# Kernel optimization log

Hardware: AMD Instinct MI355X
Metric: run time of the kernel (lower is better)

The kernel has to match this reference:

```python
import jax, jax.numpy as jnp
import numpy as np
from jax import lax

SIGMA = 1.5
KERNEL_SIZE = 11
C1 = 0.01 ** 2  # (k1 * data_range)^2 with data_range = 1.0
C2 = 0.03 ** 2


def _gaussian_kernel_1d(kernel_size: int, sigma: float) -> jnp.ndarray:
    coords = jnp.arange(kernel_size, dtype=jnp.float32) - (kernel_size - 1) / 2.0
    g = jnp.exp(-(coords ** 2) / (2.0 * sigma ** 2))
    return g / jnp.sum(g)


def _gaussian_blur(x: jnp.ndarray, g: jnp.ndarray) -> jnp.ndarray:
    """Separable depthwise Gaussian blur, VALID padding. x: [B,C,H,W], g: [k]."""
    c = x.shape[1]
    k = g.shape[0]
    dn = lax.conv_dimension_numbers(x.shape, (c, 1, k, 1), ('NCHW', 'OIHW', 'NCHW'))
    wh = jnp.broadcast_to(g.reshape(1, 1, k, 1), (c, 1, k, 1)).astype(x.dtype)
    ww = jnp.broadcast_to(g.reshape(1, 1, 1, k), (c, 1, 1, k)).astype(x.dtype)
    y = lax.conv_general_dilated(x, wh, (1, 1), 'VALID', dimension_numbers=dn, feature_group_count=c)
    y = lax.conv_general_dilated(y, ww, (1, 1), 'VALID', dimension_numbers=dn, feature_group_count=c)
    return y


def setup_inputs() -> dict:
    key = jax.random.key(0)
    k1, k2 = jax.random.split(key)
    shape = (16, 3, 512, 512)
    return {
        'input': jax.random.uniform(k1, shape, dtype=jnp.float32),
        'target': jax.random.uniform(k2, shape, dtype=jnp.float32),
    }


def reference(input, target):
    g = _gaussian_kernel_1d(KERNEL_SIZE, SIGMA)
    mu_x = _gaussian_blur(input, g)
    mu_y = _gaussian_blur(target, g)
    mu_x2 = mu_x * mu_x
    mu_y2 = mu_y * mu_y
    mu_xy = mu_x * mu_y
    var_x = _gaussian_blur(input * input, g) - mu_x2
    var_y = _gaussian_blur(target * target, g) - mu_y2
    cov_xy = _gaussian_blur(input * target, g) - mu_xy
    ssim_map = ((2.0 * mu_xy + C1) * (2.0 * cov_xy + C2)) / ((mu_x2 + mu_y2 + C1) * (var_x + var_y + C2))
    return 1.0 - jnp.mean(ssim_map)
```

## Files before the change

### kernel.cpp

```cpp
#include <hip/hip_runtime.h>

#define IH 512
#define IW 512
#define OH 502
#define OW 502
#define KS 11
#define HO 16
#define NSTRIP 32
#define NCH 48
#define NBLK (NCH * NSTRIP)
#define NT 256
#define LROW 528
#define C1f 0.0001f
#define C2f 0.0009f

__device__ __constant__ float g_w[KS] = {
    0.00102838f, 0.00759876f, 0.03600077f, 0.10936069f, 0.21300554f,
    0.26601173f, 0.21300554f, 0.10936069f, 0.03600077f, 0.00759876f,
    0.00102838f};

#define BARRIER() do {                                        \
    asm volatile("s_waitcnt lgkmcnt(0)" ::: "memory");        \
    __builtin_amdgcn_s_barrier();                             \
} while (0)

__global__ __launch_bounds__(NT, 2) void ssim_main(const float* __restrict__ x,
                                                   const float* __restrict__ y,
                                                   double* __restrict__ acc,
                                                   unsigned int* __restrict__ cnt,
                                                   float* __restrict__ out) {
    __shared__ float lds[5][2][LROW];
    __shared__ float red[4];

    const int t = threadIdx.x;
    const int ch = blockIdx.x / NSTRIP;
    const int strip = blockIdx.x % NSTRIP;
    const int r0 = strip * HO;
    const float* __restrict__ xc = x + (size_t)ch * IH * IW + 2 * t;
    const float* __restrict__ yc = y + (size_t)ch * IH * IW + 2 * t;

    float2 rx[KS], ry[KS];
#pragma unroll
    for (int i = 0; i < KS; ++i) {
        const int gr = min(r0 + i, IH - 1);
        rx[i] = *(const float2*)(xc + gr * IW);
        ry[i] = *(const float2*)(yc + gr * IW);
    }
    float2 nx0, ny0, nx1, ny1;
    {
        const int g0 = min(r0 + 11, IH - 1);
        const int g1 = min(r0 + 12, IH - 1);
        nx0 = *(const float2*)(xc + g0 * IW);
        ny0 = *(const float2*)(yc + g0 * IW);
        nx1 = *(const float2*)(xc + g1 * IW);
        ny1 = *(const float2*)(yc + g1 * IW);
    }

    float lsum = 0.f;

    for (int k = 0; k < HO / 2; ++k) {
        {
            float s0[2] = {0.f, 0.f}, s1[2] = {0.f, 0.f}, s2[2] = {0.f, 0.f};
            float s3[2] = {0.f, 0.f}, s4[2] = {0.f, 0.f};
#pragma unroll
            for (int tp = 0; tp < KS; ++tp) {
                const float w = g_w[tp];
                const float2 xv = rx[tp];
                const float2 yv = ry[tp];
                const float wx0 = w * xv.x, wx1 = w * xv.y;
                const float wy0 = w * yv.x, wy1 = w * yv.y;
                s0[0] += wx0;  s0[1] += wx1;
                s1[0] += wy0;  s1[1] += wy1;
                s2[0] = fmaf(wx0, xv.x, s2[0]);  s2[1] = fmaf(wx1, xv.y, s2[1]);
                s3[0] = fmaf(wy0, yv.x, s3[0]);  s3[1] = fmaf(wy1, yv.y, s3[1]);
                s4[0] = fmaf(wx0, yv.x, s4[0]);  s4[1] = fmaf(wx1, yv.y, s4[1]);
            }
            *(float2*)&lds[0][0][2 * t] = make_float2(s0[0], s0[1]);
            *(float2*)&lds[1][0][2 * t] = make_float2(s1[0], s1[1]);
            *(float2*)&lds[2][0][2 * t] = make_float2(s2[0], s2[1]);
            *(float2*)&lds[3][0][2 * t] = make_float2(s3[0], s3[1]);
            *(float2*)&lds[4][0][2 * t] = make_float2(s4[0], s4[1]);
        }
        {
            float s0[2] = {0.f, 0.f}, s1[2] = {0.f, 0.f}, s2[2] = {0.f, 0.f};
            float s3[2] = {0.f, 0.f}, s4[2] = {0.f, 0.f};
#pragma unroll
            for (int tp = 0; tp < KS; ++tp) {
                const float w = g_w[tp];
                const float2 xv = (tp < KS - 1) ? rx[tp + 1] : nx0;
                const float2 yv = (tp < KS - 1) ? ry[tp + 1] : ny0;
                const float wx0 = w * xv.x, wx1 = w * xv.y;
                const float wy0 = w * yv.x, wy1 = w * yv.y;
                s0[0] += wx0;  s0[1] += wx1;
                s1[0] += wy0;  s1[1] += wy1;
                s2[0] = fmaf(wx0, xv.x, s2[0]);  s2[1] = fmaf(wx1, xv.y, s2[1]);
                s3[0] = fmaf(wy0, yv.x, s3[0]);  s3[1] = fmaf(wy1, yv.y, s3[1]);
                s4[0] = fmaf(wx0, yv.x, s4[0]);  s4[1] = fmaf(wx1, yv.y, s4[1]);
            }
            *(float2*)&lds[0][1][2 * t] = make_float2(s0[0], s0[1]);
            *(float2*)&lds[1][1][2 * t] = make_float2(s1[0], s1[1]);
            *(float2*)&lds[2][1][2 * t] = make_float2(s2[0], s2[1]);
            *(float2*)&lds[3][1][2 * t] = make_float2(s3[0], s3[1]);
            *(float2*)&lds[4][1][2 * t] = make_float2(s4[0], s4[1]);
        }
        BARRIER();

#pragma unroll
        for (int i = 0; i < KS - 2; ++i) { rx[i] = rx[i + 2]; ry[i] = ry[i + 2]; }
        rx[KS - 2] = nx0; ry[KS - 2] = ny0;
        rx[KS - 1] = nx1; ry[KS - 1] = ny1;
        {
            const int g0 = min(r0 + 2 * k + 13, IH - 1);
            const int g1 = min(r0 + 2 * k + 14, IH - 1);
            nx0 = *(const float2*)(xc + g0 * IW);
            ny0 = *(const float2*)(yc + g0 * IW);
            nx1 = *(const float2*)(xc + g1 * IW);
            ny1 = *(const float2*)(yc + g1 * IW);
        }

        {
            const int rr = t >> 7;
            const int c4 = (t & 127) * 4;
            const int orow = r0 + 2 * k + rr;
            float m[5][4];
#pragma unroll
            for (int q = 0; q < 5; ++q) {
                float f[16];
#pragma unroll
                for (int a = 0; a < 4; ++a)
                    *(float4*)&f[4 * a] = *(const float4*)&lds[q][rr][c4 + 4 * a];
#pragma unroll
                for (int cc = 0; cc < 4; ++cc) {
                    float s = 0.f;
#pragma unroll
                    for (int tp = 0; tp < KS; ++tp) s = fmaf(g_w[tp], f[cc + tp], s);
                    m[q][cc] = s;
                }
            }
            if (orow < OH) {
#pragma unroll
                for (int cc = 0; cc < 4; ++cc) {
                    const int gc = c4 + cc;
                    if (gc < OW) {
                        const float mux2 = m[0][cc] * m[0][cc];
                        const float muy2 = m[1][cc] * m[1][cc];
                        const float muxy = m[0][cc] * m[1][cc];
                        const float vx = m[2][cc] - mux2;
                        const float vy = m[3][cc] - muy2;
                        const float cxy = m[4][cc] - muxy;
                        const float num = (2.f * muxy + C1f) * (2.f * cxy + C2f);
                        const float den = (mux2 + muy2 + C1f) * (vx + vy + C2f);
                        float r = __builtin_amdgcn_rcpf(den);
                        r = r * fmaf(-den, r, 2.0f);
                        lsum = fmaf(num, r, lsum);
                    }
                }
            }
        }
        BARRIER();
    }

#pragma unroll
    for (int off = 32; off > 0; off >>= 1) lsum += __shfl_down(lsum, off, 64);
    const int wave = t >> 6, lane = t & 63;
    if (lane == 0) red[wave] = lsum;
    __syncthreads();
    if (t == 0) {
        const float bs = (red[0] + red[1]) + (red[2] + red[3]);
        atomicAdd(acc, (double)bs);
        __threadfence();
        const unsigned int prev = atomicAdd(cnt, 1u);
        if (prev == (unsigned int)(NBLK - 1)) {
            const double total = atomicAdd(acc, 0.0);
            out[0] = (float)(1.0 - total / 12096192.0);
        }
    }
}

extern "C" void kernel_launch(void* const* d_in, const int* in_sizes, int n_in,
                              void* d_out, int out_size, void* d_ws, size_t ws_size,
                              hipStream_t stream) {
    const float* x = (const float*)d_in[0];
    const float* y = (const float*)d_in[1];
    float* out = (float*)d_out;
    double* acc = (double*)d_ws;
    unsigned int* cnt = (unsigned int*)((char*)d_ws + 8);

    hipMemsetAsync(d_ws, 0, 16, stream);
    ssim_main<<<NBLK, NT, 0, stream>>>(x, y, acc, cnt, out);
}
```

Before: 85.26 us.

## Give each wave a private column slab with halo to drop block barriers

Each of the four waves now owns a 128-column slab and its own LDS region. The first ten lanes also load and vertically blur a 10-column halo, so the horizontal pass reads only data written by its own wave. This lets the per-row-pair workgroup barriers become plain LDS waitcnts, removing cross-wave synchronisation stalls. In exchange there is extra halo load and compute work, divergent halo lanes, and launch bounds lowered to one block per SIMD, which allows more registers but may reduce occupancy.

```diff
diff --git a/kernel.cpp b/kernel.cpp
--- a/kernel.cpp
+++ b/kernel.cpp
@@ -10,7 +10,7 @@
 #define NCH 48
 #define NBLK (NCH * NSTRIP)
 #define NT 256
-#define LROW 528
+#define LREG 144
 #define C1f 0.0001f
 #define C2f 0.0009f
 
@@ -19,41 +19,58 @@
     0.26601173f, 0.21300554f, 0.10936069f, 0.03600077f, 0.00759876f,
     0.00102838f};
 
-#define BARRIER() do {                                        \
-    asm volatile("s_waitcnt lgkmcnt(0)" ::: "memory");        \
-    __builtin_amdgcn_s_barrier();                             \
-} while (0)
-
-__global__ __launch_bounds__(NT, 2) void ssim_main(const float* __restrict__ x,
+#define WAITLDS() asm volatile("s_waitcnt lgkmcnt(0)" ::: "memory")
+
+__global__ __launch_bounds__(NT, 1) void ssim_main(const float* __restrict__ x,
                                                    const float* __restrict__ y,
                                                    double* __restrict__ acc,
                                                    unsigned int* __restrict__ cnt,
                                                    float* __restrict__ out) {
-    __shared__ float lds[5][2][LROW];
+    __shared__ float lds[4][5][2][LREG];
     __shared__ float red[4];
 
     const int t = threadIdx.x;
+    const int w = t >> 6;
+    const int l = t & 63;
     const int ch = blockIdx.x / NSTRIP;
     const int strip = blockIdx.x % NSTRIP;
     const int r0 = strip * HO;
-    const float* __restrict__ xc = x + (size_t)ch * IH * IW + 2 * t;
-    const float* __restrict__ yc = y + (size_t)ch * IH * IW + 2 * t;
+    const int W0 = w * 128;
+    const float* __restrict__ xc = x + (size_t)ch * IH * IW;
+    const float* __restrict__ yc = y + (size_t)ch * IH * IW;
+    const int mc = W0 + 2 * l;
+    const int hc = min(W0 + 128 + l, IW - 1);
+    const bool halo = (l < 10);
 
     float2 rx[KS], ry[KS];
+    float hx[KS], hy[KS];
 #pragma unroll
     for (int i = 0; i < KS; ++i) {
         const int gr = min(r0 + i, IH - 1);
-        rx[i] = *(const float2*)(xc + gr * IW);
-        ry[i] = *(const float2*)(yc + gr * IW);
-    }
-    float2 nx0, ny0, nx1, ny1;
+        rx[i] = *(const float2*)(xc + gr * IW + mc);
+        ry[i] = *(const float2*)(yc + gr * IW + mc);
+    }
+    if (halo) {
+#pragma unroll
+        for (int i = 0; i < KS; ++i) {
+            const int gr = min(r0 + i, IH - 1);
+            hx[i] = xc[gr * IW + hc];
+            hy[i] = yc[gr * IW + hc];
+        }
+    }
+    float2 n0x, n0y, n1x, n1y;
+    float h0x = 0.f, h0y = 0.f, h1x = 0.f, h1y = 0.f;
     {
         const int g0 = min(r0 + 11, IH - 1);
         const int g1 = min(r0 + 12, IH - 1);
-        nx0 = *(const float2*)(xc + g0 * IW);
-        ny0 = *(const float2*)(yc + g0 * IW);
-        nx1 = *(const float2*)(xc + g1 * IW);
-        ny1 = *(const float2*)(yc + g1 * IW);
+        n0x = *(const float2*)(xc + g0 * IW + mc);
+        n0y = *(const float2*)(yc + g0 * IW + mc);
+        n1x = *(const float2*)(xc + g1 * IW + mc);
+        n1y = *(const float2*)(yc + g1 * IW + mc);
+        if (halo) {
+            h0x = xc[g0 * IW + hc];  h0y = yc[g0 * IW + hc];
+            h1x = xc[g1 * IW + hc];  h1y = yc[g1 * IW + hc];
+        }
     }
 
     float lsum = 0.f;
@@ -64,63 +81,93 @@
             float s3[2] = {0.f, 0.f}, s4[2] = {0.f, 0.f};
 #pragma unroll
             for (int tp = 0; tp < KS; ++tp) {
-                const float w = g_w[tp];
-                const float2 xv = rx[tp];
-                const float2 yv = ry[tp];
-                const float wx0 = w * xv.x, wx1 = w * xv.y;
-                const float wy0 = w * yv.x, wy1 = w * yv.y;
+                const float wg = g_w[tp];
+                const float2 xv = rx[tp], yv = ry[tp];
+                const float wx0 = wg * xv.x, wx1 = wg * xv.y;
+                const float wy0 = wg * yv.x, wy1 = wg * yv.y;
                 s0[0] += wx0;  s0[1] += wx1;
                 s1[0] += wy0;  s1[1] += wy1;
                 s2[0] = fmaf(wx0, xv.x, s2[0]);  s2[1] = fmaf(wx1, xv.y, s2[1]);
                 s3[0] = fmaf(wy0, yv.x, s3[0]);  s3[1] = fmaf(wy1, yv.y, s3[1]);
                 s4[0] = fmaf(wx0, yv.x, s4[0]);  s4[1] = fmaf(wx1, yv.y, s4[1]);
             }
-            *(float2*)&lds[0][0][2 * t] = make_float2(s0[0], s0[1]);
-            *(float2*)&lds[1][0][2 * t] = make_float2(s1[0], s1[1]);
-            *(float2*)&lds[2][0][2 * t] = make_float2(s2[0], s2[1]);
-            *(float2*)&lds[3][0][2 * t] = make_float2(s3[0], s3[1]);
-            *(float2*)&lds[4][0][2 * t] = make_float2(s4[0], s4[1]);
+            *(float2*)&lds[w][0][0][2 * l] = make_float2(s0[0], s0[1]);
+            *(float2*)&lds[w][1][0][2 * l] = make_float2(s1[0], s1[1]);
+            *(float2*)&lds[w][2][0][2 * l] = make_float2(s2[0], s2[1]);
+            *(float2*)&lds[w][3][0][2 * l] = make_float2(s3[0], s3[1]);
+            *(float2*)&lds[w][4][0][2 * l] = make_float2(s4[0], s4[1]);
         }
         {
             float s0[2] = {0.f, 0.f}, s1[2] = {0.f, 0.f}, s2[2] = {0.f, 0.f};
             float s3[2] = {0.f, 0.f}, s4[2] = {0.f, 0.f};
 #pragma unroll
             for (int tp = 0; tp < KS; ++tp) {
-                const float w = g_w[tp];
-                const float2 xv = (tp < KS - 1) ? rx[tp + 1] : nx0;
-                const float2 yv = (tp < KS - 1) ? ry[tp + 1] : ny0;
-                const float wx0 = w * xv.x, wx1 = w * xv.y;
-                const float wy0 = w * yv.x, wy1 = w * yv.y;
+                const float wg = g_w[tp];
+                const float2 xv = (tp < KS - 1) ? rx[tp + 1] : n0x;
+                const float2 yv = (tp < KS - 1) ? ry[tp + 1] : n0y;
+                const float wx0 = wg * xv.x, wx1 = wg * xv.y;
+                const float wy0 = wg * yv.x, wy1 = wg * yv.y;
                 s0[0] += wx0;  s0[1] += wx1;
                 s1[0] += wy0;  s1[1] += wy1;
                 s2[0] = fmaf(wx0, xv.x, s2[0]);  s2[1] = fmaf(wx1, xv.y, s2[1]);
                 s3[0] = fmaf(wy0, yv.x, s3[0]);  s3[1] = fmaf(wy1, yv.y, s3[1]);
                 s4[0] = fmaf(wx0, yv.x, s4[0]);  s4[1] = fmaf(wx1, yv.y, s4[1]);
             }
-            *(float2*)&lds[0][1][2 * t] = make_float2(s0[0], s0[1]);
-            *(float2*)&lds[1][1][2 * t] = make_float2(s1[0], s1[1]);
-            *(float2*)&lds[2][1][2 * t] = make_float2(s2[0], s2[1]);
-            *(float2*)&lds[3][1][2 * t] = make_float2(s3[0], s3[1]);
-            *(float2*)&lds[4][1][2 * t] = make_float2(s4[0], s4[1]);
-        }
-        BARRIER();
+            *(float2*)&lds[w][0][1][2 * l] = make_float2(s0[0], s0[1]);
+            *(float2*)&lds[w][1][1][2 * l] = make_float2(s1[0], s1[1]);
+            *(float2*)&lds[w][2][1][2 * l] = make_float2(s2[0], s2[1]);
+            *(float2*)&lds[w][3][1][2 * l] = make_float2(s3[0], s3[1]);
+            *(float2*)&lds[w][4][1][2 * l] = make_float2(s4[0], s4[1]);
+        }
+        if (halo) {
+            float a0 = 0, a1 = 0, a2 = 0, a3 = 0, a4 = 0;
+            float b0 = 0, b1 = 0, b2 = 0, b3 = 0, b4 = 0;
+#pragma unroll
+            for (int tp = 0; tp < KS; ++tp) {
+                const float wg = g_w[tp];
+                const float xv = hx[tp], yv = hy[tp];
+                const float wx = wg * xv, wy = wg * yv;
+                a0 += wx;  a1 += wy;
+                a2 = fmaf(wx, xv, a2);  a3 = fmaf(wy, yv, a3);  a4 = fmaf(wx, yv, a4);
+                const float xw = (tp < KS - 1) ? hx[tp + 1] : h0x;
+                const float yw = (tp < KS - 1) ? hy[tp + 1] : h0y;
+                const float vx = wg * xw, vy = wg * yw;
+                b0 += vx;  b1 += vy;
+                b2 = fmaf(vx, xw, b2);  b3 = fmaf(vy, yw, b3);  b4 = fmaf(vx, yw, b4);
+            }
+            lds[w][0][0][128 + l] = a0;  lds[w][1][0][128 + l] = a1;
+            lds[w][2][0][128 + l] = a2;  lds[w][3][0][128 + l] = a3;
+            lds[w][4][0][128 + l] = a4;
+            lds[w][0][1][128 + l] = b0;  lds[w][1][1][128 + l] = b1;
+            lds[w][2][1][128 + l] = b2;  lds[w][3][1][128 + l] = b3;
+            lds[w][4][1][128 + l] = b4;
+        }
+        WAITLDS();
 
 #pragma unroll
         for (int i = 0; i < KS - 2; ++i) { rx[i] = rx[i + 2]; ry[i] = ry[i + 2]; }
-        rx[KS - 2] = nx0; ry[KS - 2] = ny0;
-        rx[KS - 1] = nx1; ry[KS - 1] = ny1;
+        rx[KS - 2] = n0x; ry[KS - 2] = n0y;
+        rx[KS - 1] = n1x; ry[KS - 1] = n1y;
         {
             const int g0 = min(r0 + 2 * k + 13, IH - 1);
             const int g1 = min(r0 + 2 * k + 14, IH - 1);
-            nx0 = *(const float2*)(xc + g0 * IW);
-            ny0 = *(const float2*)(yc + g0 * IW);
-            nx1 = *(const float2*)(xc + g1 * IW);
-            ny1 = *(const float2*)(yc + g1 * IW);
-        }
-
-        {
-            const int rr = t >> 7;
-            const int c4 = (t & 127) * 4;
+            n0x = *(const float2*)(xc + g0 * IW + mc);
+            n0y = *(const float2*)(yc + g0 * IW + mc);
+            n1x = *(const float2*)(xc + g1 * IW + mc);
+            n1y = *(const float2*)(yc + g1 * IW + mc);
+            if (halo) {
+#pragma unroll
+                for (int i = 0; i < KS - 2; ++i) { hx[i] = hx[i + 2]; hy[i] = hy[i + 2]; }
+                hx[KS - 2] = h0x; hy[KS - 2] = h0y;
+                hx[KS - 1] = h1x; hy[KS - 1] = h1y;
+                h0x = xc[g0 * IW + hc];  h0y = yc[g0 * IW + hc];
+                h1x = xc[g1 * IW + hc];  h1y = yc[g1 * IW + hc];
+            }
+        }
+
+        {
+            const int rr = l >> 5;
+            const int c4 = 4 * (l & 31);
             const int orow = r0 + 2 * k + rr;
             float m[5][4];
 #pragma unroll
@@ -128,7 +175,7 @@
                 float f[16];
 #pragma unroll
                 for (int a = 0; a < 4; ++a)
-                    *(float4*)&f[4 * a] = *(const float4*)&lds[q][rr][c4 + 4 * a];
+                    *(float4*)&f[4 * a] = *(const float4*)&lds[w][q][rr][c4 + 4 * a];
 #pragma unroll
                 for (int cc = 0; cc < 4; ++cc) {
                     float s = 0.f;
@@ -140,8 +187,8 @@
             if (orow < OH) {
 #pragma unroll
                 for (int cc = 0; cc < 4; ++cc) {
-                    const int gc = c4 + cc;
-                    if (gc < OW) {
+                    const int oc = W0 + c4 + cc;
+                    if (oc < OW) {
                         const float mux2 = m[0][cc] * m[0][cc];
                         const float muy2 = m[1][cc] * m[1][cc];
                         const float muxy = m[0][cc] * m[1][cc];
@@ -157,13 +204,12 @@
                 }
             }
         }
-        BARRIER();
+        WAITLDS();
     }
 
 #pragma unroll
     for (int off = 32; off > 0; off >>= 1) lsum += __shfl_down(lsum, off, 64);
-    const int wave = t >> 6, lane = t & 63;
-    if (lane == 0) red[wave] = lsum;
+    if (l == 0) red[w] = lsum;
     __syncthreads();
     if (t == 0) {
         const float bs = (red[0] + red[1]) + (red[2] + red[3]);
```

Result: slower. 100.5 us (+17.8%).
